# Kernel tuning notes

Measured on AMD Instinct MI355X. Metric: run time of the kernel, lower is better.

Reference implementation:

```python
import jax, jax.numpy as jnp
import numpy as np

EPS = 1e-5
TRANSITION_BINS = 16

def layernorm(x, w, b):
    m = jnp.mean(x, axis=-1, keepdims=True)
    v = jnp.var(x, axis=-1, keepdims=True)
    return (x - m) / jnp.sqrt(v + EPS) * w + b

def freq_mask(Fbins, cutoff, trans):
    # static (python) construction of the progressive-training cutoff mask
    c = min(int(cutoff), Fbins)
    if c >= Fbins:
        return None
    tr = min(trans, c)
    mask = np.ones(Fbins, dtype=np.float32)
    if tr > 0:
        t = np.linspace(0.0, 1.0, tr, dtype=np.float32)
        mask[c - tr:c] = 0.5 * (1.0 + np.cos(np.pi * t))
    mask[c:] = 0.0
    return jnp.asarray(mask)

def setup_inputs() -> dict:
    key = jax.random.key(0)
    ks = jax.random.split(key, 8)
    B, T, C, K = 4, 4096, 1024, 1024
    n_fft = 1
    while n_fft < T + K - 1:
        n_fft *= 2
    Fbins = n_fft // 2 + 1  # 4097
    H = 2 * C
    return {
        "x": jax.random.normal(ks[0], (B, T, C), jnp.float32),
        "kernel": jax.random.normal(ks[1], (K,), jnp.float32) * 0.001,
        "gain": jnp.ones((C,), jnp.float32),
        "gate_freq_logits": jnp.full((Fbins,), 2.0, jnp.float32),
        "gate_ctx_w": jax.random.normal(ks[2], (C, C), jnp.float32) * 0.01,
        "gate_ctx_b": jnp.full((C,), 2.0, jnp.float32),
        "ln_w": jnp.ones((C,), jnp.float32),
        "ln_b": jnp.zeros((C,), jnp.float32),
        "ffn_ln_w": jnp.ones((C,), jnp.float32),
        "ffn_ln_b": jnp.zeros((C,), jnp.float32),
        "ffn_w1": jax.random.normal(ks[3], (C, H), jnp.float32) * 0.01,
        "ffn_b1": jnp.zeros((H,), jnp.float32),
        "ffn_w2": jax.random.normal(ks[4], (H, C), jnp.float32) * 0.01,
        "ffn_b2": jnp.zeros((C,), jnp.float32),
        "cutoff": 2048,
    }

def reference(x, kernel, gain, gate_freq_logits, gate_ctx_w, gate_ctx_b,
              ln_w, ln_b, ffn_ln_w, ffn_ln_b, ffn_w1, ffn_b1, ffn_w2, ffn_b2,
              cutoff):
    B, T, C = x.shape
    K = kernel.shape[0]
    n_fft = 1
    while n_fft < T + K - 1:
        n_fft *= 2
    Fbins = n_fft // 2 + 1

    residual = x
    xn = layernorm(x, ln_w, ln_b)

    # causal FFT convolution with learned one-sided kernel
    k_freq = jnp.fft.rfft(kernel, n=n_fft)                 # [Fbins] complex
    x_freq = jnp.fft.rfft(xn, n=n_fft, axis=1)             # [B,Fbins,C]

    # static + context-dependent frequency/channel gates
    g_freq = jax.nn.sigmoid(gate_freq_logits[:Fbins])      # [Fbins]
    pooled = jnp.mean(xn, axis=1)                          # [B,C]
    g_ctx = jax.nn.sigmoid(pooled @ gate_ctx_w + gate_ctx_b)  # [B,C]

    y_freq = x_freq * (k_freq * g_freq)[None, :, None] \
                    * (gain[None, None, :] * g_ctx[:, None, :])

    m = freq_mask(Fbins, cutoff, TRANSITION_BINS)
    if m is not None:
        y_freq = y_freq * m[None, :, None]

    y = jnp.fft.irfft(y_freq, n=n_fft, axis=1)[:, :T, :]   # [B,T,C]
    x2 = residual + y  # dropout is identity at eval

    # FFN sublayer
    ff_in = layernorm(x2, ffn_ln_w, ffn_ln_b)
    h = jax.nn.gelu(ff_in @ ffn_w1 + ffn_b1, approximate=False)
    return x2 + (h @ ffn_w2 + ffn_b2)
```

## Files before the change

### kernel.cpp

```cpp
#include <hip/hip_runtime.h>
#include <hip/hip_bf16.h>
#include <cstdint>
#include <cstddef>

#define DEV static __device__ __forceinline__

typedef __hip_bfloat16 hb;
typedef __bf16 bf16x8 __attribute__((ext_vector_type(8)));
typedef float f32x4 __attribute__((ext_vector_type(4)));
typedef __attribute__((address_space(1))) unsigned int as1_u32;
typedef __attribute__((address_space(3))) unsigned int as3_u32;

constexpr int B_ = 4, T_ = 4096, C_ = 1024, NFFT = 8192, FB = 4097, H_ = 2048;
constexpr int BT_ = B_ * T_;
constexpr float EPS_ = 1e-5f;
constexpr int TRANS_ = 16;
constexpr int TW_S1 = 0;
constexpr int TW_S2 = 240;
constexpr int TW_UNT = 4080;
constexpr int TW_TOTAL = 6128;

DEV void gload16(const void* gsrc, void* ldst) {
  __builtin_amdgcn_global_load_lds((as1_u32*)gsrc, (as3_u32*)ldst, 16, 0, 0);
}

DEV unsigned short bfbits(float f) {
  hb h = __float2bfloat16(f);
  return __builtin_bit_cast(unsigned short, h);
}
DEV float bf2f(unsigned short u) {
  unsigned int x = ((unsigned int)u) << 16;
  return __builtin_bit_cast(float, x);
}

__global__ __launch_bounds__(256) void build_tw(float2* __restrict__ tw) {
  const int i = blockIdx.x * 256 + threadIdx.x;
  if (i < 240) {
    const int pos = i / 15, q = i % 15 + 1;
    float sn, cs;
    sincospif((float)(pos * q) * (1.0f / 128.0f), &sn, &cs);
    tw[i] = make_float2(cs, sn);
  } else if (i < 4080) {
    const int j = i - 240;
    const int pos = j / 15, q = j % 15 + 1;
    float sn, cs;
    sincospif((float)(pos * q) * (1.0f / 2048.0f), &sn, &cs);
    tw[i] = make_float2(cs, sn);
  } else if (i < TW_TOTAL) {
    const int k = i - TW_UNT;
    float sn, cs;
    sincospif((float)k * (1.0f / 4096.0f), &sn, &cs);
    tw[i] = make_float2(cs, sn);
  }
}

__global__ __launch_bounds__(256) void build_keff(const float* __restrict__ kern,
                                                  const float* __restrict__ logits,
                                                  const int* __restrict__ cutp,
                                                  float* __restrict__ keff) {
  const int f = blockIdx.x;
  const int tid = threadIdx.x;
  float sr = 0.f, si = 0.f;
#pragma unroll
  for (int u = 0; u < 4; u++) {
    const int k = tid + u * 256;
    const float kv = kern[k];
    const int m = (f * k) & (NFFT - 1);
    float sn, cs;
    sincospif((float)m * (1.0f / 4096.0f), &sn, &cs);
    sr = fmaf(kv, cs, sr);
    si = fmaf(kv, -sn, si);
  }
#pragma unroll
  for (int o = 32; o > 0; o >>= 1) { sr += __shfl_xor(sr, o); si += __shfl_xor(si, o); }
  __shared__ float redr[4], redi[4];
  if ((tid & 63) == 0) { redr[tid >> 6] = sr; redi[tid >> 6] = si; }
  __syncthreads();
  if (tid == 0) {
    float kr = redr[0] + redr[1] + redr[2] + redr[3];
    float ki = redi[0] + redi[1] + redi[2] + redi[3];
    const float g = 1.0f / (1.0f + expf(-logits[f]));
    int cc = *cutp; if (cc > FB) cc = FB;
    float msk = 1.0f;
    if (cc < FB) {
      int tr = TRANS_ < cc ? TRANS_ : cc;
      if (f >= cc) msk = 0.0f;
      else if (f >= cc - tr) {
        int i = f - (cc - tr);
        int den = (tr > 1) ? (tr - 1) : 1;
        msk = 0.5f * (1.0f + cospif((float)i / (float)den));
      }
    }
    const float gm = g * msk;
    keff[2 * f] = kr * gm;
    keff[2 * f + 1] = ki * gm;
  }
}

__global__ __launch_bounds__(256) void ln_stats(const float* __restrict__ x,
                                                float* __restrict__ mu,
                                                float* __restrict__ rs) {
  const int row = blockIdx.x * 4 + (threadIdx.x >> 6);
  const int l = threadIdx.x & 63;
  const float4* p = (const float4*)(x + (size_t)row * C_);
  float s = 0.f, sq = 0.f;
#pragma unroll
  for (int u = 0; u < 4; u++) {
    float4 v = p[l + 64 * u];
    s += v.x + v.y + v.z + v.w;
    sq += v.x * v.x + v.y * v.y + v.z * v.z + v.w * v.w;
  }
#pragma unroll
  for (int o = 32; o > 0; o >>= 1) { s += __shfl_xor(s, o); sq += __shfl_xor(sq, o); }
  if (l == 0) {
    float m = s * (1.0f / C_);
    float var = sq * (1.0f / C_) - m * m;
    mu[row] = m;
    rs[row] = rsqrtf(var + EPS_);
  }
}

__global__ __launch_bounds__(256) void ln_apply_transpose(const float* __restrict__ x,
                                                          const float* __restrict__ mu,
                                                          const float* __restrict__ rs,
                                                          const float* __restrict__ lw,
                                                          const float* __restrict__ lb,
                                                          unsigned short* __restrict__ xtb,
                                                          float* __restrict__ partials) {
  __shared__ float tile[32 * 129];
  const int t0 = blockIdx.x * 32;
  const int c0 = blockIdx.y * 128;
  const int b = blockIdx.z;
  const int tid = threadIdx.x;
#pragma unroll
  for (int u = 0; u < 16; u++) {
    const int idx = tid + u * 256;
    const int row = idx >> 7, col = idx & 127;
    const int t = t0 + row;
    const float v = x[((size_t)(b * T_ + t)) * C_ + c0 + col];
    tile[row * 129 + col] = (v - mu[b * T_ + t]) * rs[b * T_ + t] * lw[c0 + col] + lb[c0 + col];
  }
  __syncthreads();
#pragma unroll
  for (int u = 0; u < 16; u++) {
    const int idx = tid + u * 256;
    const int cc = idx >> 5, tt = idx & 31;
    xtb[((size_t)(b * C_ + c0 + cc)) * T_ + t0 + tt] = bfbits(tile[tt * 129 + cc]);
  }
  if (tid < 128) {
    float s = 0.f;
#pragma unroll
    for (int tt = 0; tt < 32; tt++) s += tile[tt * 129 + tid];
    partials[((size_t)(b * C_ + c0 + tid)) * (T_ / 32) + blockIdx.x] = s;
  }
}

__global__ __launch_bounds__(256) void pool_finish(const float* __restrict__ partials,
                                                   float* __restrict__ pooled) {
  const int bc = blockIdx.x * 4 + (threadIdx.x >> 6);
  const int l = threadIdx.x & 63;
  const float2 v = ((const float2*)(partials + (size_t)bc * 128))[l];
  float s = v.x + v.y;
#pragma unroll
  for (int o = 32; o > 0; o >>= 1) s += __shfl_xor(s, o);
  if (l == 0) pooled[bc] = s;
}

__global__ __launch_bounds__(256) void ctx_gate(const float* __restrict__ pooled,
                                                const float* __restrict__ W,
                                                const float* __restrict__ cb,
                                                const float* __restrict__ gain,
                                                float* __restrict__ scale) {
  const int b = blockIdx.y;
  const int c = blockIdx.x * 256 + threadIdx.x;
  __shared__ float pm[C_];
#pragma unroll
  for (int u = 0; u < 4; u++)
    pm[threadIdx.x + 256 * u] = pooled[b * C_ + threadIdx.x + 256 * u] * (1.0f / T_);
  __syncthreads();
  float a[8] = {0.f, 0.f, 0.f, 0.f, 0.f, 0.f, 0.f, 0.f};
  for (int k0 = 0; k0 < C_; k0 += 8) {
#pragma unroll
    for (int q = 0; q < 8; q++)
      a[q] = fmaf(pm[k0 + q], W[(size_t)(k0 + q) * C_ + c], a[q]);
  }
  const float z = a[0] + a[1] + a[2] + a[3] + a[4] + a[5] + a[6] + a[7] + cb[c];
  scale[b * C_ + c] = gain[c] * (1.0f / (1.0f + expf(-z)));
}

DEV int fft_addr(int i) { return i + (i >> 5) + (i >> 10); }
DEV int rev16_3(int n) { return ((n & 15) << 8) | (n & 240) | (n >> 8); }

DEV void r4ip(float (&xr)[16], float (&xi)[16], const int s0, const int s1,
              const int s2, const int s3, const float SGN) {
  const float a0r = xr[s0] + xr[s2], a0i = xi[s0] + xi[s2];
  const float d0r = xr[s0] - xr[s2], d0i = xi[s0] - xi[s2];
  const float a1r = xr[s1] + xr[s3], a1i = xi[s1] + xi[s3];
  const float d1r = xr[s1] - xr[s3], d1i = xi[s1] - xi[s3];
  xr[s0] = a0r + a1r; xi[s0] = a0i + a1i;
  xr[s2] = a0r - a1r; xi[s2] = a0i - a1i;
  xr[s1] = d0r - SGN * d1i; xi[s1] = d0i + SGN * d1r;
  xr[s3] = d0r + SGN * d1i; xi[s3] = d0i - SGN * d1r;
}

template <int INV, bool HALF>
DEV void dft16(float (&xr)[16], float (&xi)[16]) {
  constexpr float SGN = INV ? 1.0f : -1.0f;
  constexpr float C1 = 0.9238795325112867f, S1 = 0.3826834323650898f;
  constexpr float R2 = 0.7071067811865476f;
#pragma unroll
  for (int a = 0; a < 4; a++) {
    if constexpr (HALF) {
      const float ar = xr[a], ai = xi[a], br = xr[a + 4], bi = xi[a + 4];
      xr[a] = ar + br;             xi[a] = ai + bi;
      xr[a + 4] = ar - SGN * bi;   xi[a + 4] = ai + SGN * br;
      xr[a + 8] = ar - br;         xi[a + 8] = ai - bi;
      xr[a + 12] = ar + SGN * bi;  xi[a + 12] = ai - SGN * br;
    } else {
      r4ip(xr, xi, a, a + 4, a + 8, a + 12, SGN);
    }
  }
  auto tm = [&](int s, float wr, float wi) {
    const float t = xr[s] * wr - xi[s] * wi;
    xi[s] = xr[s] * wi + xi[s] * wr;
    xr[s] = t;
  };
  tm(5, C1, SGN * S1);
  tm(6, R2, SGN * R2);
  tm(7, S1, SGN * C1);
  tm(9, R2, SGN * R2);
  { const float t = -SGN * xi[10]; xi[10] = SGN * xr[10]; xr[10] = t; }
  tm(11, -R2, SGN * R2);
  tm(13, S1, SGN * C1);
  tm(14, -R2, SGN * R2);
  tm(15, -C1, -SGN * S1);
#pragma unroll
  for (int m = 0; m < 4; m++)
    r4ip(xr, xi, 4 * m + 0, 4 * m + 1, 4 * m + 2, 4 * m + 3, SGN);
}

template <int INV, int L, bool HALF>
DEV void fft_stage(float* sre, float* sim, const int g, const float2* __restrict__ twp) {
  constexpr float SGN = INV ? 1.0f : -1.0f;
  int base, pos;
  if constexpr (L == 1) { base = g << 4; pos = 0; }
  else if constexpr (L == 16) { base = ((g >> 4) << 8) | (g & 15); pos = g & 15; }
  else { base = g; pos = g; }
  float xr[16], xi[16];
#pragma unroll
  for (int q = 0; q < (HALF ? 8 : 16); q++) {
    const int idx = fft_addr(base + q * L);
    xr[q] = sre[idx]; xi[q] = sim[idx];
  }
  if constexpr (L > 1) {
    const float2* tp = twp + pos * 15;
#pragma unroll
    for (int q = 1; q < 16; q++) {
      const float2 w = tp[q - 1];
      const float wr = w.x, wi = SGN * w.y;
      const float t = xr[q] * wr - xi[q] * wi;
      xi[q] = xr[q] * wi + xi[q] * wr;
      xr[q] = t;
    }
  }
  dft16<INV, HALF>(xr, xi);
#pragma unroll
  for (int q = 0; q < 16; q++) {
    const int s = ((q & 3) << 2) | (q >> 2);
    const int idx = fft_addr(base + q * L);
    sre[idx] = xr[s]; sim[idx] = xi[s];
  }
}

__global__ __launch_bounds__(256) void fftconv(unsigned short* __restrict__ xtb,
                                               const float* __restrict__ keff,
                                               const float* __restrict__ scale,
                                               const float2* __restrict__ tw) {
  __shared__ float sre[4226];
  __shared__ float sim[4226];
  const int bc = blockIdx.x;
  const int tid = threadIdx.x;
  unsigned short* col = xtb + (size_t)bc * T_;
  const ushort2* c2 = (const ushort2*)col;
  const float2* k2 = (const float2*)keff;
  const float2* twu = tw + TW_UNT;

#pragma unroll
  for (int u = 0; u < 8; u++) {
    const int n = tid + u * 256;
    const ushort2 v = c2[n];
    const int idx = fft_addr(rev16_3(n));
    sre[idx] = bf2f(v.x); sim[idx] = bf2f(v.y);
  }
  __syncthreads();
  fft_stage<0, 1, true>(sre, sim, tid, tw);
  __syncthreads();
  fft_stage<0, 16, false>(sre, sim, tid, tw + TW_S1);
  __syncthreads();
  fft_stage<0, 256, false>(sre, sim, tid, tw + TW_S2);
  __syncthreads();

  const float s = scale[bc] * (1.0f / 4096.0f);
  float ozr[8], ozi[8], omr[8], omi[8];
#pragma unroll
  for (int u = 0; u < 8; u++) {
    const int k = tid + u * 256;
    if (k == 0) {
      const float z0r = sre[fft_addr(0)], z0i = sim[fft_addr(0)];
      const float zhr = sre[fft_addr(2048)], zhi = sim[fft_addr(2048)];
      const float X0 = z0r + z0i, XN = z0r - z0i;
      const float Y0 = X0 * keff[0] * s;
      const float YN = XN * keff[2 * 4096] * s;
      ozr[u] = 0.5f * (Y0 + YN); ozi[u] = 0.5f * (Y0 - YN);
      const float gr = keff[2 * 2048] * s, gi = keff[2 * 2048 + 1] * s;
      const float Yr = zhr * gr + zhi * gi;
      const float Yi = zhr * gi - zhi * gr;
      omr[u] = Yr; omi[u] = -Yi;
    } else {
      const int m = 4096 - k;
      const float zkr = sre[fft_addr(k)], zki = sim[fft_addr(k)];
      const float zmr = sre[fft_addr(m)], zmi = sim[fft_addr(m)];
      const float Ar = 0.5f * (zkr + zmr), Ai = 0.5f * (zki - zmi);
      const float Br = 0.5f * (zki + zmi), Bi = 0.5f * (zmr - zkr);
      const float2 wc = twu[k];
      const float cw = wc.x, sw = wc.y;
      const float Tr = Br * cw + Bi * sw, Ti = Bi * cw - Br * sw;
      const float X1r = Ar + Tr, X1i = Ai + Ti;
      const float X2r = Ar - Tr, X2i = Ti - Ai;
      const float2 g1 = k2[k], g2 = k2[m];
      const float g1r = g1.x * s, g1i = g1.y * s;
      const float g2r = g2.x * s, g2i = g2.y * s;
      const float Y1r = X1r * g1r - X1i * g1i, Y1i = X1r * g1i + X1i * g1r;
      const float Y2r = X2r * g2r - X2i * g2i, Y2i = X2r * g2i + X2i * g2r;
      const float A1r = 0.5f * (Y1r + Y2r), A1i = 0.5f * (Y1i - Y2i);
      const float Dr = 0.5f * (Y1r - Y2r), Di = 0.5f * (Y1i + Y2i);
      const float B1r = Dr * cw - Di * sw, B1i = Dr * sw + Di * cw;
      ozr[u] = A1r - B1i; ozi[u] = A1i + B1r;
      omr[u] = A1r + B1i; omi[u] = B1r - A1i;
    }
  }
  __syncthreads();
#pragma unroll
  for (int u = 0; u < 8; u++) {
    const int k = tid + u * 256;
    const int m = (k == 0) ? 2048 : 4096 - k;
    const int rk = fft_addr(rev16_3(k)), rm = fft_addr(rev16_3(m));
    sre[rk] = ozr[u]; sim[rk] = ozi[u];
    sre[rm] = omr[u]; sim[rm] = omi[u];
  }
  __syncthreads();
  fft_stage<1, 1, false>(sre, sim, tid, tw);
  __syncthreads();
  fft_stage<1, 16, false>(sre, sim, tid, tw + TW_S1);
  __syncthreads();
  fft_stage<1, 256, false>(sre, sim, tid, tw + TW_S2);
  __syncthreads();

  ushort2* o2 = (ushort2*)col;
#pragma unroll
  for (int u = 0; u < 8; u++) {
    const int n = tid + u * 256;
    o2[n] = make_ushort2(bfbits(sre[fft_addr(n)]), bfbits(sim[fft_addr(n)]));
  }
}

__global__ __launch_bounds__(256) void add_residual_transpose(const float* __restrict__ x,
                                                              const unsigned short* __restrict__ ytb,
                                                              float* __restrict__ out) {
  __shared__ float tile[32 * 129];
  const int t0 = blockIdx.x * 128;
  const int c0 = blockIdx.y * 32;
  const int b = blockIdx.z;
  const int tid = threadIdx.x;
#pragma unroll
  for (int u = 0; u < 4; u++) {
    const int idx4 = tid + u * 256;
    const int cr = idx4 >> 5, tq = idx4 & 31;
    const ushort4 v = *(const ushort4*)(ytb + ((size_t)(b * C_ + c0 + cr)) * T_ + t0 + tq * 4);
    tile[cr * 129 + tq * 4 + 0] = bf2f(v.x);
    tile[cr * 129 + tq * 4 + 1] = bf2f(v.y);
    tile[cr * 129 + tq * 4 + 2] = bf2f(v.z);
    tile[cr * 129 + tq * 4 + 3] = bf2f(v.w);
  }
  __syncthreads();
#pragma unroll
  for (int u = 0; u < 16; u++) {
    const int idx = tid + u * 256;
    const int tr = idx >> 5, cc = idx & 31;
    const size_t o = ((size_t)(b * T_ + t0 + tr)) * C_ + c0 + cc;
    out[o] = x[o] + tile[cc * 129 + tr];
  }
}

__global__ __launch_bounds__(256) void ln2_apply(const float* __restrict__ x2,
                                                 const float* __restrict__ lw,
                                                 const float* __restrict__ lb,
                                                 hb* __restrict__ outb) {
  const int row = blockIdx.x * 4 + (threadIdx.x >> 6);
  const int l = threadIdx.x & 63;
  const float4* p = (const float4*)(x2 + (size_t)row * C_);
  float4 v[4];
  float s = 0.f, sq = 0.f;
#pragma unroll
  for (int u = 0; u < 4; u++) {
    v[u] = p[l + 64 * u];
    s += v[u].x + v[u].y + v[u].z + v[u].w;
    sq += v[u].x * v[u].x + v[u].y * v[u].y + v[u].z * v[u].z + v[u].w * v[u].w;
  }
#pragma unroll
  for (int o = 32; o > 0; o >>= 1) { s += __shfl_xor(s, o); sq += __shfl_xor(sq, o); }
  const float m = s * (1.0f / C_);
  const float r = rsqrtf(sq * (1.0f / C_) - m * m + EPS_);
  ushort4* ob = (ushort4*)(outb + (size_t)row * C_);
  const float4* wp = (const float4*)lw;
  const float4* bp = (const float4*)lb;
#pragma unroll
  for (int u = 0; u < 4; u++) {
    const float4 w4 = wp[l + 64 * u], b4 = bp[l + 64 * u];
    ushort4 o4;
    o4.x = bfbits((v[u].x - m) * r * w4.x + b4.x);
    o4.y = bfbits((v[u].y - m) * r * w4.y + b4.y);
    o4.z = bfbits((v[u].z - m) * r * w4.z + b4.z);
    o4.w = bfbits((v[u].w - m) * r * w4.w + b4.w);
    ob[l + 64 * u] = o4;
  }
}

__global__ __launch_bounds__(256) void transpose_cast(const float* __restrict__ src,
                                                      hb* __restrict__ dst,
                                                      int R, int Cc) {
  __shared__ float tile[32 * 33];
  const int c0 = blockIdx.x * 32, r0 = blockIdx.y * 32;
  const int tid = threadIdx.x;
#pragma unroll
  for (int u = 0; u < 4; u++) {
    const int idx = tid + u * 256;
    const int r = idx >> 5, c = idx & 31;
    tile[r * 33 + c] = src[(size_t)(r0 + r) * Cc + c0 + c];
  }
  __syncthreads();
#pragma unroll
  for (int u = 0; u < 4; u++) {
    const int idx = tid + u * 256;
    const int c = idx >> 5, r = idx & 31;
    dst[(size_t)(c0 + c) * R + r0 + r] = __float2bfloat16(tile[r * 33 + c]);
  }
}

template <int EPI, int NG, int KG>
__global__ __launch_bounds__(256, 4) void gemm_k(const unsigned short* __restrict__ A,
                                                 const unsigned short* __restrict__ Bm,
                                                 const float* __restrict__ bias,
                                                 float* __restrict__ outf,
                                                 hb* __restrict__ outh) {
  __shared__ __align__(16) unsigned short As[128 * 64];
  __shared__ __align__(16) unsigned short Bs[128 * 64];
  constexpr int GN = NG / 128;
  const int nwg = (BT_ / 128) * GN;
  const int bid = blockIdx.x;
  const int wg = (bid & 7) * (nwg >> 3) + (bid >> 3);
  const int m0 = (wg / GN) * 128, n0 = (wg % GN) * 128;
  const int tid = threadIdx.x;
  const int r = tid >> 3, sl = tid & 7;
  const int l = tid & 63, wv = tid >> 6;
  const int wm = wv >> 1, wn = wv & 1;
  const int lr = l & 15, lq = l >> 4;

  f32x4 acc[4][4];
#pragma unroll
  for (int i = 0; i < 4; i++)
#pragma unroll
    for (int j = 0; j < 4; j++) acc[i][j] = f32x4{0.f, 0.f, 0.f, 0.f};

  for (int k0 = 0; k0 < KG; k0 += 64) {
#pragma unroll
    for (int ch = 0; ch < 4; ch++) {
      const int row = ch * 32 + r;
      const int slot = sl ^ (row & 7);
      gload16(A + (size_t)(m0 + row) * KG + k0 + slot * 8, &As[ch * 2048 + tid * 8]);
      gload16(Bm + (size_t)(n0 + row) * KG + k0 + slot * 8, &Bs[ch * 2048 + tid * 8]);
    }
    __syncthreads();
#pragma unroll
    for (int ks = 0; ks < 2; ks++) {
      bf16x8 av[4], bv[4];
#pragma unroll
      for (int i = 0; i < 4; i++) {
        const int row = wm * 64 + i * 16 + lr;
        av[i] = *reinterpret_cast<const bf16x8*>(As + row * 64 + (((ks * 4 + lq) ^ (row & 7)) * 8));
      }
#pragma unroll
      for (int j = 0; j < 4; j++) {
        const int row = wn * 64 + j * 16 + lr;
        bv[j] = *reinterpret_cast<const bf16x8*>(Bs + row * 64 + (((ks * 4 + lq) ^ (row & 7)) * 8));
      }
#pragma unroll
      for (int i = 0; i < 4; i++)
#pragma unroll
        for (int j = 0; j < 4; j++)
          acc[i][j] = __builtin_amdgcn_mfma_f32_16x16x32_bf16(av[i], bv[j], acc[i][j], 0, 0, 0);
    }
    __syncthreads();
  }

#pragma unroll
  for (int i = 0; i < 4; i++) {
#pragma unroll
    for (int j = 0; j < 4; j++) {
      const int n = n0 + wn * 64 + j * 16 + lr;
      const float bn = bias[n];
#pragma unroll
      for (int rr = 0; rr < 4; rr++) {
        const int m = m0 + wm * 64 + i * 16 + lq * 4 + rr;
        const float v = acc[i][j][rr] + bn;
        if constexpr (EPI == 0) {
          const float u = 1.5957691216f * fmaf(0.044715f * v, v * v, v);
          const float ge = v / (1.0f + __expf(-u));
          outh[(size_t)m * NG + n] = __float2bfloat16(ge);
        } else {
          outf[(size_t)m * NG + n] += v;
        }
      }
    }
  }
}

extern "C" void kernel_launch(void* const* d_in, const int* in_sizes, int n_in,
                              void* d_out, int out_size, void* d_ws, size_t ws_size,
                              hipStream_t stream) {
  (void)in_sizes; (void)n_in; (void)out_size; (void)ws_size;
  const float* x    = (const float*)d_in[0];
  const float* kern = (const float*)d_in[1];
  const float* gain = (const float*)d_in[2];
  const float* gfl  = (const float*)d_in[3];
  const float* gcw  = (const float*)d_in[4];
  const float* gcb  = (const float*)d_in[5];
  const float* lnw  = (const float*)d_in[6];
  const float* lnb  = (const float*)d_in[7];
  const float* flnw = (const float*)d_in[8];
  const float* flnb = (const float*)d_in[9];
  const float* w1   = (const float*)d_in[10];
  const float* b1   = (const float*)d_in[11];
  const float* w2   = (const float*)d_in[12];
  const float* b2   = (const float*)d_in[13];
  const int*   cut  = (const int*)d_in[14];
  float* out = (float*)d_out;

  char* ws = (char*)d_ws;
  size_t off = 0;
  auto alloc = [&](size_t bytes) -> void* {
    void* p = ws + off;
    off += (bytes + 255) & ~(size_t)255;
    return p;
  };
  unsigned short* xtb = (unsigned short*)alloc((size_t)B_ * C_ * T_ * 2);
  hb*    ffin   = (hb*)alloc((size_t)BT_ * C_ * 2);
  hb*    hbuf   = (hb*)alloc((size_t)BT_ * H_ * 2);
  hb*    w1t    = (hb*)alloc((size_t)H_ * C_ * 2);
  hb*    w2t    = (hb*)alloc((size_t)C_ * H_ * 2);
  float* keff   = (float*)alloc((size_t)FB * 2 * 4);
  float* mu     = (float*)alloc((size_t)BT_ * 4);
  float* rs     = (float*)alloc((size_t)BT_ * 4);
  float* parts  = (float*)alloc((size_t)B_ * C_ * (T_ / 32) * 4);
  float* pooled = (float*)alloc((size_t)B_ * C_ * 4);
  float* scale  = (float*)alloc((size_t)B_ * C_ * 4);
  float2* tw    = (float2*)alloc((size_t)TW_TOTAL * 8);

  build_tw<<<(TW_TOTAL + 255) / 256, 256, 0, stream>>>(tw);
  build_keff<<<FB, 256, 0, stream>>>(kern, gfl, cut, keff);
  ln_stats<<<BT_ / 4, 256, 0, stream>>>(x, mu, rs);
  ln_apply_transpose<<<dim3(T_ / 32, C_ / 128, B_), 256, 0, stream>>>(x, mu, rs, lnw, lnb, xtb, parts);
  pool_finish<<<B_ * C_ / 4, 256, 0, stream>>>(parts, pooled);
  ctx_gate<<<dim3(C_ / 256, B_), 256, 0, stream>>>(pooled, gcw, gcb, gain, scale);
  fftconv<<<B_ * C_, 256, 0, stream>>>(xtb, keff, scale, tw);
  add_residual_transpose<<<dim3(T_ / 128, C_ / 32, B_), 256, 0, stream>>>(x, xtb, out);
  ln2_apply<<<BT_ / 4, 256, 0, stream>>>(out, flnw, flnb, ffin);
  transpose_cast<<<dim3(H_ / 32, C_ / 32), 256, 0, stream>>>(w1, w1t, C_, H_);
  transpose_cast<<<dim3(C_ / 32, H_ / 32), 256, 0, stream>>>(w2, w2t, H_, C_);
  gemm_k<0, H_, C_><<<(BT_ / 128) * (H_ / 128), 256, 0, stream>>>(
      (const unsigned short*)ffin, (const unsigned short*)w1t, b1, nullptr, hbuf);
  gemm_k<1, C_, H_><<<(BT_ / 128) * (C_ / 128), 256, 0, stream>>>(
      (const unsigned short*)hbuf, (const unsigned short*)w2t, b2, out, nullptr);
}
```

Baseline: 369.7 us.

## Switch FFN GEMMs from bf16 to fp8 e4m3 MFMA with scaled weights

Quantizes the FFN LayerNorm output, hidden activations and transposed weights to fp8 e4m3, with the weights pre-scaled by 64. Both GEMMs now use the fp8 16x16x32 MFMA with a 128-wide K tile, and the scale is removed in the epilogue. This is meant to halve memory traffic and LDS footprint per K element and to use the higher fp8 matrix throughput. It costs precision through unscaled activation quantization, which may raise the numerical error against the fp32 reference.

Result: faster. 306.4 us (-17.1%).

```diff
diff --git a/kernel.cpp b/kernel.cpp
--- a/kernel.cpp
+++ b/kernel.cpp
@@ -1,12 +1,12 @@
 #include <hip/hip_runtime.h>
 #include <hip/hip_bf16.h>
+#include <hip/hip_fp8.h>
 #include <cstdint>
 #include <cstddef>
 
 #define DEV static __device__ __forceinline__
 
 typedef __hip_bfloat16 hb;
-typedef __bf16 bf16x8 __attribute__((ext_vector_type(8)));
 typedef float f32x4 __attribute__((ext_vector_type(4)));
 typedef __attribute__((address_space(1))) unsigned int as1_u32;
 typedef __attribute__((address_space(3))) unsigned int as3_u32;
@@ -19,6 +19,8 @@
 constexpr int TW_S2 = 240;
 constexpr int TW_UNT = 4080;
 constexpr int TW_TOTAL = 6128;
+constexpr float WSCALE = 64.0f;
+constexpr float INV_WS = 1.0f / 64.0f;
 
 DEV void gload16(const void* gsrc, void* ldst) {
   __builtin_amdgcn_global_load_lds((as1_u32*)gsrc, (as3_u32*)ldst, 16, 0, 0);
@@ -31,6 +33,10 @@
 DEV float bf2f(unsigned short u) {
   unsigned int x = ((unsigned int)u) << 16;
   return __builtin_bit_cast(float, x);
+}
+DEV uint8_t f2e4m3(float f) {
+  __hip_fp8_e4m3 q(f);
+  return (uint8_t)q.__x;
 }
 
 __global__ __launch_bounds__(256) void build_tw(float2* __restrict__ tw) {
@@ -395,7 +401,7 @@
 __global__ __launch_bounds__(256) void ln2_apply(const float* __restrict__ x2,
                                                  const float* __restrict__ lw,
                                                  const float* __restrict__ lb,
-                                                 hb* __restrict__ outb) {
+                                                 uint8_t* __restrict__ outq) {
   const int row = blockIdx.x * 4 + (threadIdx.x >> 6);
   const int l = threadIdx.x & 63;
   const float4* p = (const float4*)(x2 + (size_t)row * C_);
@@ -411,23 +417,23 @@
   for (int o = 32; o > 0; o >>= 1) { s += __shfl_xor(s, o); sq += __shfl_xor(sq, o); }
   const float m = s * (1.0f / C_);
   const float r = rsqrtf(sq * (1.0f / C_) - m * m + EPS_);
-  ushort4* ob = (ushort4*)(outb + (size_t)row * C_);
+  uchar4* ob = (uchar4*)(outq + (size_t)row * C_);
   const float4* wp = (const float4*)lw;
   const float4* bp = (const float4*)lb;
 #pragma unroll
   for (int u = 0; u < 4; u++) {
     const float4 w4 = wp[l + 64 * u], b4 = bp[l + 64 * u];
-    ushort4 o4;
-    o4.x = bfbits((v[u].x - m) * r * w4.x + b4.x);
-    o4.y = bfbits((v[u].y - m) * r * w4.y + b4.y);
-    o4.z = bfbits((v[u].z - m) * r * w4.z + b4.z);
-    o4.w = bfbits((v[u].w - m) * r * w4.w + b4.w);
+    uchar4 o4;
+    o4.x = f2e4m3((v[u].x - m) * r * w4.x + b4.x);
+    o4.y = f2e4m3((v[u].y - m) * r * w4.y + b4.y);
+    o4.z = f2e4m3((v[u].z - m) * r * w4.z + b4.z);
+    o4.w = f2e4m3((v[u].w - m) * r * w4.w + b4.w);
     ob[l + 64 * u] = o4;
   }
 }
 
 __global__ __launch_bounds__(256) void transpose_cast(const float* __restrict__ src,
-                                                      hb* __restrict__ dst,
+                                                      uint8_t* __restrict__ dst,
                                                       int R, int Cc) {
   __shared__ float tile[32 * 33];
   const int c0 = blockIdx.x * 32, r0 = blockIdx.y * 32;
@@ -443,18 +449,18 @@
   for (int u = 0; u < 4; u++) {
     const int idx = tid + u * 256;
     const int c = idx >> 5, r = idx & 31;
-    dst[(size_t)(c0 + c) * R + r0 + r] = __float2bfloat16(tile[r * 33 + c]);
+    dst[(size_t)(c0 + c) * R + r0 + r] = f2e4m3(tile[r * 33 + c] * WSCALE);
   }
 }
 
 template <int EPI, int NG, int KG>
-__global__ __launch_bounds__(256, 4) void gemm_k(const unsigned short* __restrict__ A,
-                                                 const unsigned short* __restrict__ Bm,
+__global__ __launch_bounds__(256, 4) void gemm_k(const uint8_t* __restrict__ A,
+                                                 const uint8_t* __restrict__ Bm,
                                                  const float* __restrict__ bias,
                                                  float* __restrict__ outf,
-                                                 hb* __restrict__ outh) {
-  __shared__ __align__(16) unsigned short As[128 * 64];
-  __shared__ __align__(16) unsigned short Bs[128 * 64];
+                                                 uint8_t* __restrict__ outq) {
+  __shared__ __align__(16) uint8_t As[128 * 128];
+  __shared__ __align__(16) uint8_t Bs[128 * 128];
   constexpr int GN = NG / 128;
   const int nwg = (BT_ / 128) * GN;
   const int bid = blockIdx.x;
@@ -472,33 +478,35 @@
 #pragma unroll
     for (int j = 0; j < 4; j++) acc[i][j] = f32x4{0.f, 0.f, 0.f, 0.f};
 
-  for (int k0 = 0; k0 < KG; k0 += 64) {
+  for (int k0 = 0; k0 < KG; k0 += 128) {
 #pragma unroll
     for (int ch = 0; ch < 4; ch++) {
       const int row = ch * 32 + r;
       const int slot = sl ^ (row & 7);
-      gload16(A + (size_t)(m0 + row) * KG + k0 + slot * 8, &As[ch * 2048 + tid * 8]);
-      gload16(Bm + (size_t)(n0 + row) * KG + k0 + slot * 8, &Bs[ch * 2048 + tid * 8]);
+      gload16(A + (size_t)(m0 + row) * KG + k0 + slot * 16, &As[ch * 4096 + tid * 16]);
+      gload16(Bm + (size_t)(n0 + row) * KG + k0 + slot * 16, &Bs[ch * 4096 + tid * 16]);
     }
     __syncthreads();
 #pragma unroll
-    for (int ks = 0; ks < 2; ks++) {
-      bf16x8 av[4], bv[4];
+    for (int kk = 0; kk < 4; kk++) {
+      const int j8 = kk * 4 + lq;
+      const int jh = j8 >> 1, jl = (j8 & 1) * 8;
+      long av[4], bv[4];
 #pragma unroll
       for (int i = 0; i < 4; i++) {
         const int row = wm * 64 + i * 16 + lr;
-        av[i] = *reinterpret_cast<const bf16x8*>(As + row * 64 + (((ks * 4 + lq) ^ (row & 7)) * 8));
+        av[i] = *reinterpret_cast<const long*>(&As[row * 128 + ((jh ^ (row & 7)) * 16) + jl]);
       }
 #pragma unroll
       for (int j = 0; j < 4; j++) {
         const int row = wn * 64 + j * 16 + lr;
-        bv[j] = *reinterpret_cast<const bf16x8*>(Bs + row * 64 + (((ks * 4 + lq) ^ (row & 7)) * 8));
+        bv[j] = *reinterpret_cast<const long*>(&Bs[row * 128 + ((jh ^ (row & 7)) * 16) + jl]);
       }
 #pragma unroll
       for (int i = 0; i < 4; i++)
 #pragma unroll
         for (int j = 0; j < 4; j++)
-          acc[i][j] = __builtin_amdgcn_mfma_f32_16x16x32_bf16(av[i], bv[j], acc[i][j], 0, 0, 0);
+          acc[i][j] = __builtin_amdgcn_mfma_f32_16x16x32_fp8_fp8(av[i], bv[j], acc[i][j], 0, 0, 0);
     }
     __syncthreads();
   }
@@ -512,11 +520,11 @@
 #pragma unroll
       for (int rr = 0; rr < 4; rr++) {
         const int m = m0 + wm * 64 + i * 16 + lq * 4 + rr;
-        const float v = acc[i][j][rr] + bn;
+        const float v = fmaf(acc[i][j][rr], INV_WS, bn);
         if constexpr (EPI == 0) {
           const float u = 1.5957691216f * fmaf(0.044715f * v, v * v, v);
           const float ge = v / (1.0f + __expf(-u));
-          outh[(size_t)m * NG + n] = __float2bfloat16(ge);
+          outq[(size_t)m * NG + n] = f2e4m3(ge);
         } else {
           outf[(size_t)m * NG + n] += v;
         }
@@ -554,10 +562,10 @@
     return p;
   };
   unsigned short* xtb = (unsigned short*)alloc((size_t)B_ * C_ * T_ * 2);
-  hb*    ffin   = (hb*)alloc((size_t)BT_ * C_ * 2);
-  hb*    hbuf   = (hb*)alloc((size_t)BT_ * H_ * 2);
-  hb*    w1t    = (hb*)alloc((size_t)H_ * C_ * 2);
-  hb*    w2t    = (hb*)alloc((size_t)C_ * H_ * 2);
+  uint8_t* ffin  = (uint8_t*)alloc((size_t)BT_ * C_);
+  uint8_t* hbuf  = (uint8_t*)alloc((size_t)BT_ * H_);
+  uint8_t* w1t   = (uint8_t*)alloc((size_t)H_ * C_);
+  uint8_t* w2t   = (uint8_t*)alloc((size_t)C_ * H_);
   float* keff   = (float*)alloc((size_t)FB * 2 * 4);
   float* mu     = (float*)alloc((size_t)BT_ * 4);
   float* rs     = (float*)alloc((size_t)BT_ * 4);
@@ -578,7 +586,7 @@
   transpose_cast<<<dim3(H_ / 32, C_ / 32), 256, 0, stream>>>(w1, w1t, C_, H_);
   transpose_cast<<<dim3(C_ / 32, H_ / 32), 256, 0, stream>>>(w2, w2t, H_, C_);
   gemm_k<0, H_, C_><<<(BT_ / 128) * (H_ / 128), 256, 0, stream>>>(
-      (const unsigned short*)ffin, (const unsigned short*)w1t, b1, nullptr, hbuf);
+      ffin, w1t, b1, nullptr, hbuf);
   gemm_k<1, C_, H_><<<(BT_ / 128) * (C_ / 128), 256, 0, stream>>>(
-      (const unsigned short*)hbuf, (const unsigned short*)w2t, b2, out, nullptr);
-}
+      hbuf, w2t, b2, out, nullptr);
+}
```
